# Optimization experiments

Hardware: AMD Instinct MI355X
Metric: run time of the kernel (lower is better)

The kernel has to match this reference:

```python
import jax, jax.numpy as jnp
import numpy as np
import math

N, M = 768, 768
QDIM = KDIM = VDIM = 512
H, HD, BD = 8, 64, 40


def mish(x):
    return x * jnp.tanh(jax.nn.softplus(x))


def _lin_params(key, out_dim, in_dim):
    w = jax.random.normal(key, (out_dim, in_dim), dtype=jnp.float32) * 0.02
    b = jnp.zeros((out_dim,), dtype=jnp.float32)
    return w, b


def setup_inputs() -> dict:
    key = jax.random.key(0)
    ks = jax.random.split(key, 12)
    q = jax.random.normal(ks[0], (N, QDIM), dtype=jnp.float32)
    k = jax.random.normal(ks[1], (M, KDIM), dtype=jnp.float32)
    v = jax.random.normal(ks[2], (M, VDIM), dtype=jnp.float32)
    bias = jax.random.normal(ks[3], (N, M, BD), dtype=jnp.float32)
    q_w, q_b = _lin_params(ks[4], H * HD, QDIM)
    k_w, k_b = _lin_params(ks[5], H * HD, KDIM)
    v_w, v_b = _lin_params(ks[6], H * HD, VDIM)
    bp_w, bp_b = _lin_params(ks[7], H * BD, BD)
    o1_w, o1_b = _lin_params(ks[8], H * HD, H * HD)
    o2_w, o2_b = _lin_params(ks[9], VDIM, H * HD)
    return {"q": q, "k": k, "v": v, "bias": bias,
            "q_w": q_w, "q_b": q_b, "k_w": k_w, "k_b": k_b,
            "v_w": v_w, "v_b": v_b, "bp_w": bp_w, "bp_b": bp_b,
            "o1_w": o1_w, "o1_b": o1_b, "o2_w": o2_w, "o2_b": o2_b}


def reference(q, k, v, bias, q_w, q_b, k_w, k_b, v_w, v_b, bp_w, bp_b, o1_w, o1_b, o2_w, o2_b):
    # QKV projections -> [H, seq, head_dim]
    qh = (q @ q_w.T + q_b).reshape(N, H, HD).transpose(1, 0, 2)
    kh = (k @ k_w.T + k_b).reshape(M, H, HD).transpose(1, 0, 2)
    vh = (v @ v_w.T + v_b).reshape(M, H, HD).transpose(1, 0, 2)
    # pairwise bias: [N, M, BD] -> [N, M, H*BD], then torch-style flat reshape to [H, N, M, BD]
    bias_p = bias @ bp_w.T + bp_b  # [N, M, H*BD]
    diffs = jnp.linalg.norm(bias_p.reshape(H, N, M, BD), axis=-1)  # [H, N, M]
    logits = jnp.einsum('hnd,hmd->hnm', qh, kh) / math.sqrt(HD) + diffs
    attn = jax.nn.softmax(logits, axis=-1)
    vals = jnp.einsum('hnm,hmd->hnd', attn, vh)  # [H, N, HD]
    vals = vals.transpose(1, 0, 2).reshape(N, H * HD)
    out = mish(vals @ o1_w.T + o1_b) @ o2_w.T + o2_b  # [N, VDIM]
    return out, bias_p
```

## Files before the change

### kernel.cpp

```cpp
#include <hip/hip_runtime.h>
#include <math.h>

#define NS   768
#define DIM  512
#define NH   8
#define HD   64
#define BD   40
#define HBD  320
#define NROWS (768*768)

typedef __bf16 bf16x8 __attribute__((ext_vector_type(8)));
typedef float  f32x4  __attribute__((ext_vector_type(4)));

union FragU {
    bf16x8 v;
    unsigned short u[8];
    uint2 d2[2];
};

__device__ inline unsigned short f2bf(float f) {
    unsigned int u = __float_as_uint(f);
    unsigned int r = (u + 0x7fffu + ((u >> 16) & 1u)) >> 16;
    return (unsigned short)r;
}
__device__ inline unsigned int pk2(float x, float y) {
    return (unsigned)f2bf(x) | ((unsigned)f2bf(y) << 16);
}

__global__ __launch_bounds__(256) void gemm_mfma(const float* __restrict__ A,
                                                 const float* __restrict__ W,
                                                 const float* __restrict__ bvec,
                                                 void* __restrict__ Cout,
                                                 int mode)
{
    __shared__ unsigned short As[64][72];
    __shared__ unsigned short Ws[64][72];

    const int t   = threadIdx.x;
    const int w   = t >> 6;
    const int l   = t & 63;
    const int c16 = l & 15;
    const int g   = l >> 4;
    const int m0  = blockIdx.x * 64;
    const int cb  = blockIdx.y * 64;

    f32x4 acc[4];
#pragma unroll
    for (int tl = 0; tl < 4; ++tl) acc[tl] = (f32x4){0.f, 0.f, 0.f, 0.f};

    for (int kc = 0; kc < DIM; kc += 64) {
        __syncthreads();
#pragma unroll
        for (int rep = 0; rep < 4; ++rep) {
            int f   = t + rep * 256;
            int row = f >> 4;
            int kk  = (f & 15) << 2;
            float4 a4 = *(const float4*)&A[(size_t)(m0 + row) * DIM + kc + kk];
            *(uint2*)&As[row][kk] = make_uint2(pk2(a4.x, a4.y), pk2(a4.z, a4.w));
            float4 w4 = *(const float4*)&W[(size_t)(cb + row) * DIM + kc + kk];
            *(uint2*)&Ws[row][kk] = make_uint2(pk2(w4.x, w4.y), pk2(w4.z, w4.w));
        }
        __syncthreads();
#pragma unroll
        for (int ks = 0; ks < 2; ++ks) {
            const int k0 = ks * 32;
            FragU bA;
            bA.d2[0] = *(const uint2*)&As[w * 16 + c16][k0 + 4 * g];
            bA.d2[1] = *(const uint2*)&As[w * 16 + c16][k0 + 16 + 4 * g];
#pragma unroll
            for (int tl = 0; tl < 4; ++tl) {
                FragU aW;
                aW.d2[0] = *(const uint2*)&Ws[tl * 16 + c16][k0 + 4 * g];
                aW.d2[1] = *(const uint2*)&Ws[tl * 16 + c16][k0 + 16 + 4 * g];
                acc[tl] = __builtin_amdgcn_mfma_f32_16x16x32_bf16(aW.v, bA.v, acc[tl], 0, 0, 0);
            }
        }
    }

    const int row = m0 + w * 16 + c16;
#pragma unroll
    for (int tl = 0; tl < 4; ++tl) {
        const int col = cb + tl * 16 + g * 4;
        float4 bb = *(const float4*)&bvec[col];
        float o[4] = {acc[tl][0] + bb.x, acc[tl][1] + bb.y,
                      acc[tl][2] + bb.z, acc[tl][3] + bb.w};
        if (mode == 3) {
#pragma unroll
            for (int rr = 0; rr < 4; ++rr)
                o[rr] = o[rr] * tanhf(log1pf(expf(o[rr])));
        }
        if (mode == 0 || mode == 3) {
            *(float4*)&((float*)Cout)[(size_t)row * DIM + col] =
                make_float4(o[0], o[1], o[2], o[3]);
        } else if (mode == 1) {
            *(uint2*)&((unsigned short*)Cout)[(size_t)row * DIM + col] =
                make_uint2(pk2(o[0], o[1]), pk2(o[2], o[3]));
        } else {
            unsigned short* p = (unsigned short*)Cout;
#pragma unroll
            for (int rr = 0; rr < 4; ++rr)
                p[(size_t)(col + rr) * NS + row] = f2bf(o[rr]);
        }
    }
}

#define OSTRIDE 321

__global__ __launch_bounds__(512) void biasp_mfma(const float* __restrict__ bias,
                                                  const float* __restrict__ bp_w,
                                                  const float* __restrict__ bp_b,
                                                  float* __restrict__ bias_p,
                                                  float* __restrict__ diffs)
{
    __shared__ unsigned short Wl[HBD * BD];
    __shared__ float Ostage[32 * OSTRIDE];

    const int t    = threadIdx.x;
    const int w    = t >> 6;
    const int l    = t & 63;
    const int c16  = l & 15;
    const int g    = l >> 4;
    const long row0 = (long)blockIdx.x * 64;

    const int wrow = (w >> 1) * 16;
    const int wcol = (w & 1) * 160;

    const long arow = row0 + wrow + c16;
    const float* ap = bias + arow * BD;
    float4 a0 = *(const float4*)(ap + g * 4);
    float4 a1 = *(const float4*)(ap + 16 + g * 4);
    float4 a2 = make_float4(0.f, 0.f, 0.f, 0.f);
    if (g < 2) a2 = *(const float4*)(ap + 32 + g * 4);

    for (int i = t; i < HBD * BD / 4; i += 512) {
        float4 w4 = ((const float4*)bp_w)[i];
        ((uint2*)Wl)[i] = make_uint2(pk2(w4.x, w4.y), pk2(w4.z, w4.w));
    }

    FragU A0, A1;
    A0.d2[0] = make_uint2(pk2(a0.x, a0.y), pk2(a0.z, a0.w));
    A0.d2[1] = make_uint2(pk2(a1.x, a1.y), pk2(a1.z, a1.w));
    A1.d2[0] = make_uint2(pk2(a2.x, a2.y), pk2(a2.z, a2.w));
    A1.d2[1] = make_uint2(0u, 0u);

    __syncthreads();

    f32x4 acc[10];
#pragma unroll
    for (int tl = 0; tl < 10; ++tl) acc[tl] = (f32x4){0.f, 0.f, 0.f, 0.f};

#pragma unroll
    for (int tl = 0; tl < 10; ++tl) {
        const int n = wcol + tl * 16 + c16;
        const uint2* wp = (const uint2*)(Wl + n * BD);
        FragU B0, B1;
        B0.d2[0] = wp[g];
        B0.d2[1] = wp[4 + g];
        B1.d2[0] = (g < 2) ? wp[8 + g] : make_uint2(0u, 0u);
        B1.d2[1] = make_uint2(0u, 0u);
        acc[tl] = __builtin_amdgcn_mfma_f32_16x16x32_bf16(B0.v, A0.v, acc[tl], 0, 0, 0);
        acc[tl] = __builtin_amdgcn_mfma_f32_16x16x32_bf16(B1.v, A1.v, acc[tl], 0, 0, 0);
    }

#pragma unroll
    for (int half = 0; half < 2; ++half) {
        __syncthreads();
        if ((wrow >> 5) == half) {
            const int lrow = (wrow & 31) + c16;
            const long brow = row0 + wrow + c16;
            float ssq[4] = {0.f, 0.f, 0.f, 0.f};
#pragma unroll
            for (int tl = 0; tl < 10; ++tl) {
                const int cbase = tl * 16 + g * 4;
                float4 bb = *(const float4*)&bp_b[wcol + cbase];
                float x0 = acc[tl][0] + bb.x;
                float x1 = acc[tl][1] + bb.y;
                float x2 = acc[tl][2] + bb.z;
                float x3 = acc[tl][3] + bb.w;
                f32x4 sv = {x0, x1, x2, x3};
                *(f32x4*)&Ostage[lrow * OSTRIDE + wcol + cbase] = sv;
                float s = x0 * x0 + x1 * x1 + x2 * x2 + x3 * x3;
                ssq[0] += (cbase < 40) ? s : 0.f;
                ssq[1] += (cbase >= 40 && cbase < 80) ? s : 0.f;
                ssq[2] += (cbase >= 80 && cbase < 120) ? s : 0.f;
                ssq[3] += (cbase >= 120) ? s : 0.f;
            }
#pragma unroll
            for (int c = 0; c < 4; ++c) {
                ssq[c] += __shfl_xor(ssq[c], 16);
                ssq[c] += __shfl_xor(ssq[c], 32);
            }
            float v = (g == 0) ? ssq[0] : (g == 1) ? ssq[1] : (g == 2) ? ssq[2] : ssq[3];
            diffs[brow * 8 + (w & 1) * 4 + g] = sqrtf(v);
        }
        __syncthreads();
        float* dst = bias_p + (row0 + half * 32) * HBD;
#pragma unroll
        for (int i = 0; i < 5; ++i) {
            const int f4 = t + i * 512;
            const int fl = f4 * 4;
            const int r  = fl / 320;
            const int c  = fl - r * 320;
            f32x4 sv = *(const f32x4*)&Ostage[r * OSTRIDE + c];
            *(f32x4*)&dst[fl] = sv;
        }
    }
}

__global__ __launch_bounds__(256) void attn_mfma(const unsigned short* __restrict__ Qb,
                                                 const unsigned short* __restrict__ Kb,
                                                 const unsigned short* __restrict__ Vt,
                                                 const float* __restrict__ diffs,
                                                 float* __restrict__ vals)
{
    __shared__ float Lacc[4][64][17];
    __shared__ float Lm[4][16];
    __shared__ float Ll[4][16];

    const int t   = threadIdx.x;
    const int wv  = t >> 6;
    const int l   = t & 63;
    const int c16 = l & 15;
    const int g   = l >> 4;
    const int h   = blockIdx.y;
    const int n0  = blockIdx.x * 16;

    const unsigned short* qrow = Qb + (size_t)(n0 + c16) * DIM + h * HD;
    FragU Qf[2];
#pragma unroll
    for (int kh = 0; kh < 2; ++kh) {
        Qf[kh].d2[0] = *(const uint2*)(qrow + 4 * g + 32 * kh);
        Qf[kh].d2[1] = *(const uint2*)(qrow + 16 + 4 * g + 32 * kh);
    }

    float m_run = -1e30f, l_run = 0.f;
    f32x4 acc[4];
#pragma unroll
    for (int dt = 0; dt < 4; ++dt) acc[dt] = (f32x4){0.f, 0.f, 0.f, 0.f};

    for (int ti = 0; ti < 3; ++ti) {
        const int kb = (wv * 3 + ti) * 64;

        f32x4 s[4];
#pragma unroll
        for (int kt = 0; kt < 4; ++kt) s[kt] = (f32x4){0.f, 0.f, 0.f, 0.f};
#pragma unroll
        for (int kh = 0; kh < 2; ++kh) {
#pragma unroll
            for (int kt = 0; kt < 4; ++kt) {
                const unsigned short* krow = Kb + (size_t)(kb + kt * 16 + c16) * DIM + h * HD;
                FragU Kf;
                Kf.d2[0] = *(const uint2*)(krow + 4 * g + 32 * kh);
                Kf.d2[1] = *(const uint2*)(krow + 16 + 4 * g + 32 * kh);
                s[kt] = __builtin_amdgcn_mfma_f32_16x16x32_bf16(Kf.v, Qf[kh].v, s[kt], 0, 0, 0);
            }
        }

        const float* dbase = diffs + (size_t)h * 589824 + (size_t)(n0 + c16) * 768 + kb;
        float mx = -1e30f;
#pragma unroll
        for (int kt = 0; kt < 4; ++kt) {
            float4 d4 = *(const float4*)(dbase + kt * 16 + 4 * g);
            float dd[4] = {d4.x, d4.y, d4.z, d4.w};
#pragma unroll
            for (int r = 0; r < 4; ++r) {
                float x = s[kt][r] * 0.125f + dd[r];
                s[kt][r] = x;
                mx = fmaxf(mx, x);
            }
        }
        mx = fmaxf(mx, __shfl_xor(mx, 16));
        mx = fmaxf(mx, __shfl_xor(mx, 32));
        const float m_new = fmaxf(m_run, mx);
        const float scale = __expf(m_run - m_new);

        float psum = 0.f;
#pragma unroll
        for (int kt = 0; kt < 4; ++kt)
#pragma unroll
            for (int r = 0; r < 4; ++r) {
                float e = __expf(s[kt][r] - m_new);
                s[kt][r] = e;
                psum += e;
            }
        psum += __shfl_xor(psum, 16);
        psum += __shfl_xor(psum, 32);
        l_run = l_run * scale + psum;
        m_run = m_new;
#pragma unroll
        for (int dt = 0; dt < 4; ++dt)
#pragma unroll
            for (int r = 0; r < 4; ++r) acc[dt][r] *= scale;

        FragU Pf[2];
#pragma unroll
        for (int kh = 0; kh < 2; ++kh)
#pragma unroll
            for (int j = 0; j < 8; ++j)
                Pf[kh].u[j] = f2bf(s[2 * kh + (j >> 2)][j & 3]);

#pragma unroll
        for (int kh = 0; kh < 2; ++kh) {
#pragma unroll
            for (int dt = 0; dt < 4; ++dt) {
                const unsigned short* vrow =
                    Vt + (size_t)(h * HD + dt * 16 + c16) * NS + kb + 32 * kh + 4 * g;
                FragU Vf;
                Vf.d2[0] = *(const uint2*)(vrow);
                Vf.d2[1] = *(const uint2*)(vrow + 16);
                acc[dt] = __builtin_amdgcn_mfma_f32_16x16x32_bf16(Pf[kh].v, Vf.v, acc[dt], 0, 0, 0);
            }
        }
    }

#pragma unroll
    for (int dt = 0; dt < 4; ++dt)
#pragma unroll
        for (int r = 0; r < 4; ++r) Lacc[wv][l][dt * 4 + r] = acc[dt][r];
    if (g == 0) { Lm[wv][c16] = m_run; Ll[wv][c16] = l_run; }
    __syncthreads();

#pragma unroll
    for (int r = 0; r < 4; ++r) {
        const int qr = 4 * g + r;
        float M = fmaxf(fmaxf(Lm[0][qr], Lm[1][qr]), fmaxf(Lm[2][qr], Lm[3][qr]));
        float Lsum = 0.f, a = 0.f;
#pragma unroll
        for (int w2 = 0; w2 < 4; ++w2) {
            float e = __expf(Lm[w2][qr] - M);
            Lsum += Ll[w2][qr] * e;
            a += Lacc[w2][l][wv * 4 + r] * e;
        }
        vals[(size_t)(n0 + qr) * DIM + h * HD + wv * 16 + c16] = a / Lsum;
    }
}

extern "C" void kernel_launch(void* const* d_in, const int* in_sizes, int n_in,
                              void* d_out, int out_size, void* d_ws, size_t ws_size,
                              hipStream_t stream)
{
    const float* q    = (const float*)d_in[0];
    const float* k    = (const float*)d_in[1];
    const float* v    = (const float*)d_in[2];
    const float* bias = (const float*)d_in[3];
    const float* q_w  = (const float*)d_in[4];
    const float* q_b  = (const float*)d_in[5];
    const float* k_w  = (const float*)d_in[6];
    const float* k_b  = (const float*)d_in[7];
    const float* v_w  = (const float*)d_in[8];
    const float* v_b  = (const float*)d_in[9];
    const float* bp_w = (const float*)d_in[10];
    const float* bp_b = (const float*)d_in[11];
    const float* o1_w = (const float*)d_in[12];
    const float* o1_b = (const float*)d_in[13];
    const float* o2_w = (const float*)d_in[14];
    const float* o2_b = (const float*)d_in[15];

    float* out    = (float*)d_out;
    float* bias_p = (float*)d_out + 393216;

    float* ws    = (float*)d_ws;
    unsigned short* Qb = (unsigned short*)(ws);
    unsigned short* Kb = (unsigned short*)(ws + 393216);
    unsigned short* Vt = (unsigned short*)(ws + 786432);
    float* vals  = ws + 1179648;
    float* mid   = ws + 1572864;
    float* diffs = ws + 1966080;

    dim3 gg(12, 8), gb(256);
    gemm_mfma<<<gg, gb, 0, stream>>>(q, q_w, q_b, Qb, 1);
    gemm_mfma<<<gg, gb, 0, stream>>>(k, k_w, k_b, Kb, 1);
    gemm_mfma<<<gg, gb, 0, stream>>>(v, v_w, v_b, Vt, 2);
    biasp_mfma<<<dim3(NROWS / 64), dim3(512), 0, stream>>>(bias, bp_w, bp_b, bias_p, diffs);
    attn_mfma<<<dim3(48, NH), gb, 0, stream>>>(Qb, Kb, Vt, diffs, vals);
    gemm_mfma<<<gg, gb, 0, stream>>>(vals, o1_w, o1_b, mid, 3);
    gemm_mfma<<<gg, gb, 0, stream>>>(mid, o2_w, o2_b, out, 0);
}
```

Before: 301.6 us.

## Fuse QKV projection GEMMs into bias projection kernel as extra blocks

The three separate QKV projection launches are merged into the bias-projection kernel. The first 288 blocks each compute a 64x64 tile of Q, K or V with MFMA, and the remaining blocks run the existing bias_p/diffs path, with shared memory unioned between the two roles. This removes three kernel launches and lets the small GEMMs overlap with the bandwidth-bound bias projection. In exchange the QKV GEMM now uses a new 512-thread tiling, and occupancy is bounded by the larger shared-memory footprint of the union.

```diff
diff --git a/kernel.cpp b/kernel.cpp
--- a/kernel.cpp
+++ b/kernel.cpp
@@ -8,6 +8,8 @@
 #define BD   40
 #define HBD  320
 #define NROWS (768*768)
+#define OSTRIDE 321
+#define QKV_BLKS 288
 
 typedef __bf16 bf16x8 __attribute__((ext_vector_type(8)));
 typedef float  f32x4  __attribute__((ext_vector_type(4)));
@@ -104,26 +106,99 @@
     }
 }
 
-#define OSTRIDE 321
-
-__global__ __launch_bounds__(512) void biasp_mfma(const float* __restrict__ bias,
-                                                  const float* __restrict__ bp_w,
-                                                  const float* __restrict__ bp_b,
-                                                  float* __restrict__ bias_p,
-                                                  float* __restrict__ diffs)
+struct SMemG { unsigned short As[64][72]; unsigned short Ws[64][72]; };
+struct SMemB { unsigned short Wl[HBD * BD]; float Ostage[32 * OSTRIDE]; };
+union SMemU { SMemG g; SMemB b; };
+
+__global__ __launch_bounds__(512) void qkv_biasp(
+    const float* __restrict__ q, const float* __restrict__ k, const float* __restrict__ v,
+    const float* __restrict__ q_w, const float* __restrict__ k_w, const float* __restrict__ v_w,
+    const float* __restrict__ q_b, const float* __restrict__ k_b, const float* __restrict__ v_b,
+    unsigned short* __restrict__ Qb, unsigned short* __restrict__ Kb, unsigned short* __restrict__ Vt,
+    const float* __restrict__ bias, const float* __restrict__ bp_w, const float* __restrict__ bp_b,
+    float* __restrict__ bias_p, float* __restrict__ diffs)
 {
-    __shared__ unsigned short Wl[HBD * BD];
-    __shared__ float Ostage[32 * OSTRIDE];
-
-    const int t    = threadIdx.x;
-    const int w    = t >> 6;
-    const int l    = t & 63;
-    const int c16  = l & 15;
-    const int g    = l >> 4;
-    const long row0 = (long)blockIdx.x * 64;
-
-    const int wrow = (w >> 1) * 16;
-    const int wcol = (w & 1) * 160;
+    __shared__ SMemU sm;
+
+    const int t   = threadIdx.x;
+    const int wv  = t >> 6;
+    const int l   = t & 63;
+    const int c16 = l & 15;
+    const int g   = l >> 4;
+
+    if (blockIdx.x < QKV_BLKS) {
+        const int sub   = blockIdx.x;
+        const int which = sub / 96;
+        const int rem   = sub - which * 96;
+        const int m0    = (rem % 12) * 64;
+        const int cb    = (rem / 12) * 64;
+        const float* A  = (which == 0) ? q   : (which == 1) ? k   : v;
+        const float* W  = (which == 0) ? q_w : (which == 1) ? k_w : v_w;
+        const float* Bv = (which == 0) ? q_b : (which == 1) ? k_b : v_b;
+
+        const int wr = wv >> 1;
+        const int wc = wv & 1;
+
+        f32x4 acc[2];
+        acc[0] = (f32x4){0.f, 0.f, 0.f, 0.f};
+        acc[1] = (f32x4){0.f, 0.f, 0.f, 0.f};
+
+        for (int kc = 0; kc < DIM; kc += 64) {
+            __syncthreads();
+#pragma unroll
+            for (int rep = 0; rep < 2; ++rep) {
+                int f   = t + rep * 512;
+                int row = f >> 4;
+                int kk  = (f & 15) << 2;
+                float4 a4 = *(const float4*)&A[(size_t)(m0 + row) * DIM + kc + kk];
+                *(uint2*)&sm.g.As[row][kk] = make_uint2(pk2(a4.x, a4.y), pk2(a4.z, a4.w));
+                float4 w4 = *(const float4*)&W[(size_t)(cb + row) * DIM + kc + kk];
+                *(uint2*)&sm.g.Ws[row][kk] = make_uint2(pk2(w4.x, w4.y), pk2(w4.z, w4.w));
+            }
+            __syncthreads();
+#pragma unroll
+            for (int ks = 0; ks < 2; ++ks) {
+                const int k0 = ks * 32;
+                FragU bA;
+                bA.d2[0] = *(const uint2*)&sm.g.As[wr * 16 + c16][k0 + 4 * g];
+                bA.d2[1] = *(const uint2*)&sm.g.As[wr * 16 + c16][k0 + 16 + 4 * g];
+#pragma unroll
+                for (int tl = 0; tl < 2; ++tl) {
+                    FragU aW;
+                    aW.d2[0] = *(const uint2*)&sm.g.Ws[wc * 32 + tl * 16 + c16][k0 + 4 * g];
+                    aW.d2[1] = *(const uint2*)&sm.g.Ws[wc * 32 + tl * 16 + c16][k0 + 16 + 4 * g];
+                    acc[tl] = __builtin_amdgcn_mfma_f32_16x16x32_bf16(aW.v, bA.v, acc[tl], 0, 0, 0);
+                }
+            }
+        }
+
+        const int row = m0 + wr * 16 + c16;
+#pragma unroll
+        for (int tl = 0; tl < 2; ++tl) {
+            const int col = cb + wc * 32 + tl * 16 + g * 4;
+            float4 bb = *(const float4*)&Bv[col];
+            float o0 = acc[tl][0] + bb.x;
+            float o1 = acc[tl][1] + bb.y;
+            float o2 = acc[tl][2] + bb.z;
+            float o3 = acc[tl][3] + bb.w;
+            if (which < 2) {
+                unsigned short* p = (which == 0) ? Qb : Kb;
+                *(uint2*)&p[(size_t)row * DIM + col] =
+                    make_uint2(pk2(o0, o1), pk2(o2, o3));
+            } else {
+                Vt[(size_t)(col + 0) * NS + row] = f2bf(o0);
+                Vt[(size_t)(col + 1) * NS + row] = f2bf(o1);
+                Vt[(size_t)(col + 2) * NS + row] = f2bf(o2);
+                Vt[(size_t)(col + 3) * NS + row] = f2bf(o3);
+            }
+        }
+        return;
+    }
+
+    const long row0 = (long)(blockIdx.x - QKV_BLKS) * 64;
+    const int  w    = wv;
+    const int  wrow = (w >> 1) * 16;
+    const int  wcol = (w & 1) * 160;
 
     const long arow = row0 + wrow + c16;
     const float* ap = bias + arow * BD;
@@ -134,7 +209,7 @@
 
     for (int i = t; i < HBD * BD / 4; i += 512) {
         float4 w4 = ((const float4*)bp_w)[i];
-        ((uint2*)Wl)[i] = make_uint2(pk2(w4.x, w4.y), pk2(w4.z, w4.w));
+        ((uint2*)sm.b.Wl)[i] = make_uint2(pk2(w4.x, w4.y), pk2(w4.z, w4.w));
     }
 
     FragU A0, A1;
@@ -152,7 +227,7 @@
 #pragma unroll
     for (int tl = 0; tl < 10; ++tl) {
         const int n = wcol + tl * 16 + c16;
-        const uint2* wp = (const uint2*)(Wl + n * BD);
+        const uint2* wp = (const uint2*)(sm.b.Wl + n * BD);
         FragU B0, B1;
         B0.d2[0] = wp[g];
         B0.d2[1] = wp[4 + g];
@@ -178,7 +253,7 @@
                 float x2 = acc[tl][2] + bb.z;
                 float x3 = acc[tl][3] + bb.w;
                 f32x4 sv = {x0, x1, x2, x3};
-                *(f32x4*)&Ostage[lrow * OSTRIDE + wcol + cbase] = sv;
+                *(f32x4*)&sm.b.Ostage[lrow * OSTRIDE + wcol + cbase] = sv;
                 float s = x0 * x0 + x1 * x1 + x2 * x2 + x3 * x3;
                 ssq[0] += (cbase < 40) ? s : 0.f;
                 ssq[1] += (cbase >= 40 && cbase < 80) ? s : 0.f;
@@ -190,8 +265,8 @@
                 ssq[c] += __shfl_xor(ssq[c], 16);
                 ssq[c] += __shfl_xor(ssq[c], 32);
             }
-            float v = (g == 0) ? ssq[0] : (g == 1) ? ssq[1] : (g == 2) ? ssq[2] : ssq[3];
-            diffs[brow * 8 + (w & 1) * 4 + g] = sqrtf(v);
+            float vq = (g == 0) ? ssq[0] : (g == 1) ? ssq[1] : (g == 2) ? ssq[2] : ssq[3];
+            diffs[brow * 8 + (w & 1) * 4 + g] = sqrtf(vq);
         }
         __syncthreads();
         float* dst = bias_p + (row0 + half * 32) * HBD;
@@ -201,7 +276,7 @@
             const int fl = f4 * 4;
             const int r  = fl / 320;
             const int c  = fl - r * 320;
-            f32x4 sv = *(const f32x4*)&Ostage[r * OSTRIDE + c];
+            f32x4 sv = *(const f32x4*)&sm.b.Ostage[r * OSTRIDE + c];
             *(f32x4*)&dst[fl] = sv;
         }
     }
@@ -368,10 +443,9 @@
     float* diffs = ws + 1966080;
 
     dim3 gg(12, 8), gb(256);
-    gemm_mfma<<<gg, gb, 0, stream>>>(q, q_w, q_b, Qb, 1);
-    gemm_mfma<<<gg, gb, 0, stream>>>(k, k_w, k_b, Kb, 1);
-    gemm_mfma<<<gg, gb, 0, stream>>>(v, v_w, v_b, Vt, 2);
-    biasp_mfma<<<dim3(NROWS / 64), dim3(512), 0, stream>>>(bias, bp_w, bp_b, bias_p, diffs);
+    qkv_biasp<<<dim3(QKV_BLKS + NROWS / 64), dim3(512), 0, stream>>>(
+        q, k, v, q_w, k_w, v_w, q_b, k_b, v_b, Qb, Kb, Vt,
+        bias, bp_w, bp_b, bias_p, diffs);
     attn_mfma<<<dim3(48, NH), gb, 0, stream>>>(Qb, Kb, Vt, diffs, vals);
     gemm_mfma<<<gg, gb, 0, stream>>>(vals, o1_w, o1_b, mid, 3);
     gemm_mfma<<<gg, gb, 0, stream>>>(mid, o2_w, o2_b, out, 0);
```

New measurement: 260.0 us, median of 2. -13.8%, faster.
